# Kernel tuning notes

Hardware: AMD Instinct MI355X
Metric: run time of the kernel (lower is better)

Reference implementation:

```python
import jax, jax.numpy as jnp
import numpy as np

D_MODEL = 1024
NUM_EXPERTS = 64
TOP_K = 2
TEMPERATURE = 1.0


def setup_inputs() -> dict:
    key = jax.random.key(0)
    k1, k2, k3, k4 = jax.random.split(key, 4)
    mh_output = jax.random.normal(k1, (8, 4096, D_MODEL), dtype=jnp.float32)
    noise = jax.random.normal(k2, (8, 4096, NUM_EXPERTS), dtype=jnp.float32)  # randn_like sample, externalized
    # nn.Linear weights: shape [out, in], init normal(0, 0.02); biases zero
    W_route = jax.random.normal(k3, (NUM_EXPERTS, D_MODEL), dtype=jnp.float32) * 0.02
    b_route = jnp.zeros((NUM_EXPERTS,), dtype=jnp.float32)
    W_noise = jax.random.normal(k4, (NUM_EXPERTS, D_MODEL), dtype=jnp.float32) * 0.02
    b_noise = jnp.zeros((NUM_EXPERTS,), dtype=jnp.float32)
    return {"mh_output": mh_output, "noise": noise, "W_route": W_route,
            "b_route": b_route, "W_noise": W_noise, "b_noise": b_noise}


def reference(mh_output, noise, W_route, b_route, W_noise, b_noise):
    # logits = topkroute_linear(mh_output); noise_logits = noise_linear(mh_output)
    logits = jnp.einsum('bsd,ed->bse', mh_output, W_route) + b_route
    noise_logits = jnp.einsum('bsd,ed->bse', mh_output, W_noise) + b_noise
    # noisy logits = logits + temperature * randn * softplus(noise_logits)
    noisy = logits + TEMPERATURE * noise * jax.nn.softplus(noise_logits)
    # top-k, scatter into -inf, softmax  ==  softmax over top-k values scattered into zeros
    top_vals, indices = jax.lax.top_k(noisy, TOP_K)          # [b, s, k]
    probs_k = jax.nn.softmax(top_vals, axis=-1)              # softmax(-inf elsewhere) -> 0 elsewhere
    one_hot = jax.nn.one_hot(indices, NUM_EXPERTS, dtype=noisy.dtype)  # [b, s, k, E]
    router_output = jnp.sum(one_hot * probs_k[..., None], axis=-2)     # [b, s, E]
    return router_output, indices
```

## Files before the change

### kernel.cpp

```cpp
#include <hip/hip_runtime.h>
#include <hip/hip_bf16.h>
#include <math.h>


#define T_TOKENS 32768
#define D_MODEL  1024
#define NE       64
#define NCOL     128
#define M_TILE   64
#define NCHUNK   32
#define RING_D   4
#define CS_LD    68
#define OUT_IDX_BASE ((size_t)T_TOKENS * NE)
#define W_ELEMS  (NCOL * D_MODEL)

typedef short  bf16x8  __attribute__((ext_vector_type(8)));
typedef float  floatx4 __attribute__((ext_vector_type(4)));
typedef const __attribute__((address_space(1))) unsigned int gu32;
typedef __attribute__((address_space(3))) unsigned int lu32;

__device__ __forceinline__ float softplus_f(float x) {
    return fmaxf(x, 0.f) + log1pf(expf(-fabsf(x)));
}

__device__ __forceinline__ void cvt8(const float4 a, const float4 b,
                                     int4* hi, int4* lo) {
    float v[8] = {a.x, a.y, a.z, a.w, b.x, b.y, b.z, b.w};
    int hw[4], lw[4];
    #pragma unroll
    for (int p = 0; p < 4; ++p) {
        float2 f2 = make_float2(v[2 * p], v[2 * p + 1]);
        __hip_bfloat162 h2 = __float22bfloat162_rn(f2);
        int u; __builtin_memcpy(&u, &h2, 4);
        float h0 = __uint_as_float(((unsigned)u) << 16);
        float h1 = __uint_as_float(((unsigned)u) & 0xFFFF0000u);
        float2 l2 = make_float2(v[2 * p] - h0, v[2 * p + 1] - h1);
        __hip_bfloat162 L2 = __float22bfloat162_rn(l2);
        int ul; __builtin_memcpy(&ul, &L2, 4);
        hw[p] = u; lw[p] = ul;
    }
    *hi = make_int4(hw[0], hw[1], hw[2], hw[3]);
    *lo = make_int4(lw[0], lw[1], lw[2], lw[3]);
}

__device__ __forceinline__ void cvt8r(const float4 a, const float4 b,
                                      bf16x8* hi, bf16x8* lo) {
    int4 h, l;
    cvt8(a, b, &h, &l);
    __builtin_memcpy(hi, &h, 16);
    __builtin_memcpy(lo, &l, 16);
}

__global__ __launch_bounds__(256) void prepack_w(
    const float* __restrict__ Wr, const float* __restrict__ Wn,
    short* __restrict__ Bh, short* __restrict__ Bl)
{
    int g   = blockIdx.x * 256 + threadIdx.x;
    int n   = g & 15;
    int kg  = (g >> 4) & 127;
    int t2  = g >> 11;
    int col = t2 * 16 + n;
    const float* src = (col < NE ? Wr + (size_t)col * D_MODEL
                                 : Wn + (size_t)(col - NE) * D_MODEL) + kg * 8;
    float4 a = *(const float4*)src;
    float4 b = *(const float4*)(src + 4);
    int4 hi, lo;
    cvt8(a, b, &hi, &lo);
    *(int4*)(Bh + (size_t)g * 8) = hi;
    *(int4*)(Bl + (size_t)g * 8) = lo;
}

__global__ __launch_bounds__(256, 2) void router_mfma(
    const float* __restrict__ A,
    const float* __restrict__ noise,
    const float* __restrict__ br,
    const float* __restrict__ bn,
    const short* __restrict__ Bh,
    const short* __restrict__ Bl,
    float* __restrict__ out)
{
    __shared__ __align__(16) float ringA[RING_D * M_TILE * 32];
    __shared__ float Cs[M_TILE * CS_LD];
    __shared__ float s_p1[M_TILE], s_p2[M_TILE];
    __shared__ int   s_e1[M_TILE], s_e2[M_TILE];

    const int tid  = threadIdx.x;
    const int lane = tid & 63;
    const int wid  = tid >> 6;
    const int n16  = lane & 15;
    const int quad = lane >> 4;
    const int m0   = blockIdx.x * M_TILE;

    const int rlo = lane >> 3;
    const int csw = ((lane & 7) ^ rlo) * 4;
    const int j0  = 2 * wid;
    const float* srcA0 = A + (size_t)(m0 + j0 * 8 + rlo) * D_MODEL + csw;
    const float* srcA1 = A + (size_t)(m0 + j0 * 8 + 8 + rlo) * D_MODEL + csw;

    const int sw0 = (((quad * 32 +  0) ^ ((n16 & 7) << 4)) >> 2);
    const int sw1 = (((quad * 32 + 16) ^ ((n16 & 7) << 4)) >> 2);

    const short* pBhR = Bh + ((size_t)(wid * 128 + quad) * 16 + n16) * 8;
    const short* pBlR = Bl + ((size_t)(wid * 128 + quad) * 16 + n16) * 8;
    const short* pBhN = Bh + ((size_t)((4 + wid) * 128 + quad) * 16 + n16) * 8;
    const short* pBlN = Bl + ((size_t)((4 + wid) * 128 + quad) * 16 + n16) * 8;

#define DMA_CHUNK(KC_) do {                                                   \
        const int b_ = (KC_) & (RING_D - 1);                                  \
        __builtin_amdgcn_global_load_lds(                                     \
            (gu32*)(srcA0 + (KC_) * 32),                                      \
            (lu32*)(ringA + b_ * (M_TILE * 32) + j0 * 256), 16, 0, 0);        \
        __builtin_amdgcn_global_load_lds(                                     \
            (gu32*)(srcA1 + (KC_) * 32),                                      \
            (lu32*)(ringA + b_ * (M_TILE * 32) + (j0 + 1) * 256), 16, 0, 0);  \
    } while (0)

    floatx4 acc[4][2];
    #pragma unroll
    for (int i = 0; i < 4; ++i) { acc[i][0] = (floatx4)0.f; acc[i][1] = (floatx4)0.f; }

    DMA_CHUNK(0);
    DMA_CHUNK(1);
    DMA_CHUNK(2);
    bf16x8 bhR = *(const bf16x8*)(pBhR);
    bf16x8 blR = *(const bf16x8*)(pBlR);
    bf16x8 bhN = *(const bf16x8*)(pBhN);
    bf16x8 blN = *(const bf16x8*)(pBlN);

    for (int kc = 0; kc < NCHUNK; ++kc) {
        const int buf = kc & (RING_D - 1);

        __builtin_amdgcn_sched_barrier(0);
        if (kc < NCHUNK - 2)       asm volatile("s_waitcnt vmcnt(4)" ::: "memory");
        else if (kc == NCHUNK - 2) asm volatile("s_waitcnt vmcnt(2)" ::: "memory");
        else                       asm volatile("s_waitcnt vmcnt(0)" ::: "memory");
        __builtin_amdgcn_s_barrier();
        __builtin_amdgcn_sched_barrier(0);

        if (kc + RING_D - 1 < NCHUNK) DMA_CHUNK(kc + RING_D - 1);

        const int on = (kc + 1 < NCHUNK ? kc + 1 : kc) * 512;
        bf16x8 nbhR = *(const bf16x8*)(pBhR + on);
        bf16x8 nblR = *(const bf16x8*)(pBlR + on);
        bf16x8 nbhN = *(const bf16x8*)(pBhN + on);
        bf16x8 nblN = *(const bf16x8*)(pBlN + on);

        float4 fa[4], fb[4];
        #pragma unroll
        for (int mf = 0; mf < 4; ++mf) {
            const float* p = &ringA[buf * (M_TILE * 32) + (mf * 16 + n16) * 32];
            fa[mf] = *(const float4*)(p + sw0);
            fb[mf] = *(const float4*)(p + sw1);
        }

        #pragma unroll
        for (int mf = 0; mf < 4; ++mf) {
            bf16x8 ah, al;
            cvt8r(fa[mf], fb[mf], &ah, &al);
            acc[mf][0] = __builtin_amdgcn_mfma_f32_16x16x32_bf16(ah, bhR, acc[mf][0], 0, 0, 0);
            acc[mf][0] = __builtin_amdgcn_mfma_f32_16x16x32_bf16(ah, blR, acc[mf][0], 0, 0, 0);
            acc[mf][0] = __builtin_amdgcn_mfma_f32_16x16x32_bf16(al, bhR, acc[mf][0], 0, 0, 0);
            acc[mf][1] = __builtin_amdgcn_mfma_f32_16x16x32_bf16(ah, bhN, acc[mf][1], 0, 0, 0);
            acc[mf][1] = __builtin_amdgcn_mfma_f32_16x16x32_bf16(ah, blN, acc[mf][1], 0, 0, 0);
            acc[mf][1] = __builtin_amdgcn_mfma_f32_16x16x32_bf16(al, bhN, acc[mf][1], 0, 0, 0);
        }

        bhR = nbhR; blR = nblR; bhN = nbhN; blN = nblN;
    }
#undef DMA_CHUNK

    {
        int e = wid * 16 + n16;
        float brv = br[e], bnv = bn[e];
        #pragma unroll
        for (int mf = 0; mf < 4; ++mf)
            #pragma unroll
            for (int rr = 0; rr < 4; ++rr) {
                int t = mf * 16 + quad * 4 + rr;
                float nz    = noise[(size_t)(m0 + t) * NE + e];
                float route = acc[mf][0][rr] + brv;
                float nl    = acc[mf][1][rr] + bnv;
                Cs[t * CS_LD + e] = fmaf(nz, softplus_f(nl), route);
            }
    }
    __syncthreads();

    if (tid < M_TILE) {
        const int t = tid;
        float v1 = -INFINITY, v2 = -INFINITY;
        int e1 = 0, e2 = 0;
        #pragma unroll
        for (int e4 = 0; e4 < 16; ++e4) {
            float4 q = *(const float4*)&Cs[t * CS_LD + e4 * 4];
            float qa[4] = {q.x, q.y, q.z, q.w};
            #pragma unroll
            for (int c = 0; c < 4; ++c) {
                float v = qa[c];
                int e = e4 * 4 + c;
                if (v > v1) { v2 = v1; e2 = e1; v1 = v; e1 = e; }
                else if (v > v2) { v2 = v; e2 = e; }
            }
        }
        float ex = expf(v2 - v1);
        float denom = 1.f + ex;
        s_p1[t] = 1.f / denom;
        s_p2[t] = ex / denom;
        s_e1[t] = e1;
        s_e2[t] = e2;
        float2 iv = make_float2((float)e1, (float)e2);
        *(float2*)(out + OUT_IDX_BASE + (size_t)(m0 + t) * 2) = iv;
    }
    __syncthreads();

    #pragma unroll
    for (int i = 0; i < 4; ++i) {
        int gi = i * 256 + tid;
        int t  = gi >> 4;
        int e0 = (gi & 15) * 4;
        float p1 = s_p1[t], p2 = s_p2[t];
        int   e1 = s_e1[t], e2 = s_e2[t];
        float4 v;
        v.x = (e0 + 0 == e1) ? p1 : ((e0 + 0 == e2) ? p2 : 0.f);
        v.y = (e0 + 1 == e1) ? p1 : ((e0 + 1 == e2) ? p2 : 0.f);
        v.z = (e0 + 2 == e1) ? p1 : ((e0 + 2 == e2) ? p2 : 0.f);
        v.w = (e0 + 3 == e1) ? p1 : ((e0 + 3 == e2) ? p2 : 0.f);
        *(float4*)(out + (size_t)(m0 + t) * NE + e0) = v;
    }
}

extern "C" void kernel_launch(void* const* d_in, const int* in_sizes, int n_in,
                              void* d_out, int out_size, void* d_ws, size_t ws_size,
                              hipStream_t stream) {
    const float* A     = (const float*)d_in[0];
    const float* noise = (const float*)d_in[1];
    const float* Wr    = (const float*)d_in[2];
    const float* br    = (const float*)d_in[3];
    const float* Wn    = (const float*)d_in[4];
    const float* bn    = (const float*)d_in[5];
    float* out = (float*)d_out;

    short* Bh = (short*)d_ws;
    short* Bl = Bh + W_ELEMS;

    prepack_w<<<dim3(W_ELEMS / 8 / 256), dim3(256), 0, stream>>>(Wr, Wn, Bh, Bl);
    router_mfma<<<dim3(T_TOKENS / M_TILE), dim3(256), 0, stream>>>(A, noise, br, bn, Bh, Bl, out);
}
```

Measured before the change: 236.8 us.

## Prefetch B fragments two chunks ahead and drop LDS XOR swizzle

Deepens the weight-fragment prefetch from one to two k-chunks ahead, issuing those global loads before the wait and barrier. The vmcnt wait counts are retuned so the DMA ring still completes in time. The XOR swizzle on the A tile in LDS is also removed in favour of plain linear addressing. The deeper prefetch hides more load latency but costs extra registers, and dropping the swizzle may bring back LDS bank conflicts on the float4 reads.

```diff
diff --git a/kernel.cpp b/kernel.cpp
--- a/kernel.cpp
+++ b/kernel.cpp
@@ -92,13 +92,10 @@
     const int m0   = blockIdx.x * M_TILE;
 
     const int rlo = lane >> 3;
-    const int csw = ((lane & 7) ^ rlo) * 4;
+    const int c4  = (lane & 7) * 4;
     const int j0  = 2 * wid;
-    const float* srcA0 = A + (size_t)(m0 + j0 * 8 + rlo) * D_MODEL + csw;
-    const float* srcA1 = A + (size_t)(m0 + j0 * 8 + 8 + rlo) * D_MODEL + csw;
-
-    const int sw0 = (((quad * 32 +  0) ^ ((n16 & 7) << 4)) >> 2);
-    const int sw1 = (((quad * 32 + 16) ^ ((n16 & 7) << 4)) >> 2);
+    const float* srcA0 = A + (size_t)(m0 + j0 * 8 + rlo) * D_MODEL + c4;
+    const float* srcA1 = A + (size_t)(m0 + j0 * 8 + 8 + rlo) * D_MODEL + c4;
 
     const short* pBhR = Bh + ((size_t)(wid * 128 + quad) * 16 + n16) * 8;
     const short* pBlR = Bl + ((size_t)(wid * 128 + quad) * 16 + n16) * 8;
@@ -122,50 +119,61 @@
     DMA_CHUNK(0);
     DMA_CHUNK(1);
     DMA_CHUNK(2);
-    bf16x8 bhR = *(const bf16x8*)(pBhR);
-    bf16x8 blR = *(const bf16x8*)(pBlR);
-    bf16x8 bhN = *(const bf16x8*)(pBhN);
-    bf16x8 blN = *(const bf16x8*)(pBlN);
-
+    bf16x8 b0hR = *(const bf16x8*)(pBhR);
+    bf16x8 b0lR = *(const bf16x8*)(pBlR);
+    bf16x8 b0hN = *(const bf16x8*)(pBhN);
+    bf16x8 b0lN = *(const bf16x8*)(pBlN);
+    bf16x8 b1hR = *(const bf16x8*)(pBhR + 512);
+    bf16x8 b1lR = *(const bf16x8*)(pBlR + 512);
+    bf16x8 b1hN = *(const bf16x8*)(pBhN + 512);
+    bf16x8 b1lN = *(const bf16x8*)(pBlN + 512);
+
+    #pragma unroll 1
     for (int kc = 0; kc < NCHUNK; ++kc) {
         const int buf = kc & (RING_D - 1);
 
+        bf16x8 b2hR, b2lR, b2hN, b2lN;
+        if (kc + 2 < NCHUNK) {
+            const int o = (kc + 2) * 512;
+            b2hR = *(const bf16x8*)(pBhR + o);
+            b2lR = *(const bf16x8*)(pBlR + o);
+            b2hN = *(const bf16x8*)(pBhN + o);
+            b2lN = *(const bf16x8*)(pBlN + o);
+        }
         __builtin_amdgcn_sched_barrier(0);
-        if (kc < NCHUNK - 2)       asm volatile("s_waitcnt vmcnt(4)" ::: "memory");
-        else if (kc == NCHUNK - 2) asm volatile("s_waitcnt vmcnt(2)" ::: "memory");
-        else                       asm volatile("s_waitcnt vmcnt(0)" ::: "memory");
+
+        if (kc == 0)            asm volatile("s_waitcnt vmcnt(8)"  ::: "memory");
+        else if (kc == 1)       asm volatile("s_waitcnt vmcnt(10)" ::: "memory");
+        else if (kc < NCHUNK-2) asm volatile("s_waitcnt vmcnt(12)" ::: "memory");
+        else if (kc == NCHUNK-2)asm volatile("s_waitcnt vmcnt(4)"  ::: "memory");
+        else                    asm volatile("s_waitcnt vmcnt(0)"  ::: "memory");
         __builtin_amdgcn_s_barrier();
         __builtin_amdgcn_sched_barrier(0);
 
-        if (kc + RING_D - 1 < NCHUNK) DMA_CHUNK(kc + RING_D - 1);
-
-        const int on = (kc + 1 < NCHUNK ? kc + 1 : kc) * 512;
-        bf16x8 nbhR = *(const bf16x8*)(pBhR + on);
-        bf16x8 nblR = *(const bf16x8*)(pBlR + on);
-        bf16x8 nbhN = *(const bf16x8*)(pBhN + on);
-        bf16x8 nblN = *(const bf16x8*)(pBlN + on);
+        if (kc + 3 < NCHUNK) DMA_CHUNK(kc + 3);
 
         float4 fa[4], fb[4];
         #pragma unroll
         for (int mf = 0; mf < 4; ++mf) {
-            const float* p = &ringA[buf * (M_TILE * 32) + (mf * 16 + n16) * 32];
-            fa[mf] = *(const float4*)(p + sw0);
-            fb[mf] = *(const float4*)(p + sw1);
+            const float* p = &ringA[buf * (M_TILE * 32) + (mf * 16 + n16) * 32 + quad * 8];
+            fa[mf] = *(const float4*)(p);
+            fb[mf] = *(const float4*)(p + 4);
         }
 
         #pragma unroll
         for (int mf = 0; mf < 4; ++mf) {
             bf16x8 ah, al;
             cvt8r(fa[mf], fb[mf], &ah, &al);
-            acc[mf][0] = __builtin_amdgcn_mfma_f32_16x16x32_bf16(ah, bhR, acc[mf][0], 0, 0, 0);
-            acc[mf][0] = __builtin_amdgcn_mfma_f32_16x16x32_bf16(ah, blR, acc[mf][0], 0, 0, 0);
-            acc[mf][0] = __builtin_amdgcn_mfma_f32_16x16x32_bf16(al, bhR, acc[mf][0], 0, 0, 0);
-            acc[mf][1] = __builtin_amdgcn_mfma_f32_16x16x32_bf16(ah, bhN, acc[mf][1], 0, 0, 0);
-            acc[mf][1] = __builtin_amdgcn_mfma_f32_16x16x32_bf16(ah, blN, acc[mf][1], 0, 0, 0);
-            acc[mf][1] = __builtin_amdgcn_mfma_f32_16x16x32_bf16(al, bhN, acc[mf][1], 0, 0, 0);
-        }
-
-        bhR = nbhR; blR = nblR; bhN = nbhN; blN = nblN;
+            acc[mf][0] = __builtin_amdgcn_mfma_f32_16x16x32_bf16(ah, b0hR, acc[mf][0], 0, 0, 0);
+            acc[mf][0] = __builtin_amdgcn_mfma_f32_16x16x32_bf16(ah, b0lR, acc[mf][0], 0, 0, 0);
+            acc[mf][0] = __builtin_amdgcn_mfma_f32_16x16x32_bf16(al, b0hR, acc[mf][0], 0, 0, 0);
+            acc[mf][1] = __builtin_amdgcn_mfma_f32_16x16x32_bf16(ah, b0hN, acc[mf][1], 0, 0, 0);
+            acc[mf][1] = __builtin_amdgcn_mfma_f32_16x16x32_bf16(ah, b0lN, acc[mf][1], 0, 0, 0);
+            acc[mf][1] = __builtin_amdgcn_mfma_f32_16x16x32_bf16(al, b0hN, acc[mf][1], 0, 0, 0);
+        }
+
+        b0hR = b1hR; b0lR = b1lR; b0hN = b1hN; b0lN = b1lN;
+        b1hR = b2hR; b1lR = b2lR; b1hN = b2hN; b1lN = b2lN;
     }
 #undef DMA_CHUNK
 
```

Result: no change. 234.3 us (-1.0%).
